# Performance work log

Hardware: AMD Instinct MI355X
Metric: run time of the kernel (lower is better)

## Reference

```python
import jax, jax.numpy as jnp
import numpy as np

TOPK = 8
NOISE_EPS = 0.01
_SQRT2 = np.sqrt(2.0).astype(np.float32)

def _norm_cdf(v):
    return 0.5 * (1.0 + jax.lax.erf(v / _SQRT2))

def setup_inputs() -> dict:
    key = jax.random.key(0)
    k1, k2, k3, k4 = jax.random.split(key, 4)
    B, D, E = 16384, 4096, 64
    return {
        "x": jax.random.normal(k1, (B, D), dtype=jnp.float32),
        "w_gate": jax.random.normal(k2, (D, E), dtype=jnp.float32) * 0.02,
        "w_noise": jax.random.normal(k3, (D, E), dtype=jnp.float32) * 0.02,
        "noise": jax.random.normal(k4, (B, E), dtype=jnp.float32),
    }

def reference(x, w_gate, w_noise, noise):
    B = x.shape[0]
    clean_logits = x @ w_gate                                   # [B, E]
    noise_stddev = jax.nn.softplus(x @ w_noise) + NOISE_EPS      # [B, E]
    noisy_logits = clean_logits + noise * noise_stddev           # [B, E]
    # NOTE: original applies softmax BEFORE topk (probabilities, not logits)
    probs = jax.nn.softmax(noisy_logits, axis=1)                 # [B, E]
    top_logits, top_indices = jax.lax.top_k(probs, TOPK + 1)     # [B, k+1]
    top_k_gates = jax.nn.softmax(top_logits[:, :TOPK], axis=1)   # [B, k]
    rows = jnp.arange(B)[:, None]
    gates = jnp.zeros_like(probs).at[rows, top_indices[:, :TOPK]].set(top_k_gates)
    # _prob_in_top_k: thresholds are the (topk)-th and (topk-1)-th top probs
    thr_in = top_logits[:, TOPK:TOPK + 1]                        # [B, 1]
    thr_out = top_logits[:, TOPK - 1:TOPK]                       # [B, 1]
    is_in = noisy_logits > thr_in                                # (faithful: raw noisy vs prob threshold)
    prob_if_in = _norm_cdf((clean_logits - thr_in) / noise_stddev)
    prob_if_out = _norm_cdf((clean_logits - thr_out) / noise_stddev)
    load = jnp.where(is_in, prob_if_in, prob_if_out).sum(axis=0)  # [E]
    return gates, load
```

## Files before the change

kernel.cpp:

```cpp
#include <hip/hip_runtime.h>
#include <math.h>

#define BB 16384
#define DD 4096
#define EE 64
#define TK 8

typedef __attribute__((ext_vector_type(8))) short s16x8;
typedef __attribute__((ext_vector_type(4))) float f32x4;

__device__ inline unsigned pack_hi2(float a, float b) {
    return (__float_as_uint(a) >> 16) | (__float_as_uint(b) & 0xFFFF0000u);
}
__device__ inline float hi_part(float a) {
    return __uint_as_float(__float_as_uint(a) & 0xFFFF0000u);
}

__global__ __launch_bounds__(256, 1)
void prep_w(const float* __restrict__ wg, const float* __restrict__ wn,
            char* __restrict__ wsB)
{
    __shared__ float Wtmp[64 * 132];
    const int t  = threadIdx.x;
    const int kc = blockIdx.x;

#pragma unroll
    for (int i = 0; i < 8; ++i) {
        int fid = t + i * 256;
        int m   = fid >> 10;
        int id  = fid & 1023;
        int kk  = id >> 4;
        int n4  = id & 15;
        const float* src = (m ? wn : wg) + (size_t)(kc * 64 + kk) * EE + n4 * 4;
        float4 v = *(const float4*)src;
        *(float4*)&Wtmp[kk * 132 + m * 64 + n4 * 4] = v;
    }
    __syncthreads();

#pragma unroll
    for (int i = 0; i < 4; ++i) {
        int id  = t + i * 256;
        int sub = id >> 9;
        int nt  = (id >> 6) & 7;
        int ln  = id & 63;
        int n   = nt * 16 + (ln & 15);
        int k0  = sub * 32 + (ln >> 4) * 8;
        float f[8];
#pragma unroll
        for (int j = 0; j < 8; ++j) f[j] = Wtmp[(k0 + j) * 132 + n];
        uint4 h, l;
        h.x = pack_hi2(f[0], f[1]); h.y = pack_hi2(f[2], f[3]);
        h.z = pack_hi2(f[4], f[5]); h.w = pack_hi2(f[6], f[7]);
        l.x = pack_hi2(f[0] - hi_part(f[0]), f[1] - hi_part(f[1]));
        l.y = pack_hi2(f[2] - hi_part(f[2]), f[3] - hi_part(f[3]));
        l.z = pack_hi2(f[4] - hi_part(f[4]), f[5] - hi_part(f[5]));
        l.w = pack_hi2(f[6] - hi_part(f[6]), f[7] - hi_part(f[7]));
        size_t base = (size_t)kc * 32768;
        *(uint4*)(wsB + base + (size_t)(((sub * 2 + 0) * 8 + nt) * 64 + ln) * 16) = h;
        *(uint4*)(wsB + base + (size_t)(((sub * 2 + 1) * 8 + nt) * 64 + ln) * 16) = l;
    }
}

__global__ __launch_bounds__(512, 1)
void moe_mfma(const float* __restrict__ x,
              const float* __restrict__ noise,
              const char* __restrict__ wsB,
              float* __restrict__ gates,
              float* __restrict__ load)
{
    __shared__ uint4 Afrag[1024];
    __shared__ uint4 Bfrag[2048];
    __shared__ float Ls[64 * 132];
    __shared__ float red[512];

    const int tid  = threadIdx.x;
    const int w    = tid >> 6;
    const int lane = tid & 63;
    const int wm   = w >> 1;
    const int wn   = w & 1;
    const int rb   = blockIdx.x * 64;

    const int srow  = tid >> 3;
    const int skg   = tid & 7;
    const int ssub  = skg >> 2;
    const int sq    = skg & 3;
    const int slane = sq * 16 + (srow & 15);
    const int smt   = srow >> 4;
    const int aoff_hi = ((ssub * 2 + 0) * 4 + smt) * 64 + slane;
    const int aoff_lo = ((ssub * 2 + 1) * 4 + smt) * 64 + slane;
    const float* xrow = x + (size_t)(rb + srow) * DD + skg * 8;

    f32x4 acc[4];
#pragma unroll
    for (int nt = 0; nt < 4; ++nt) acc[nt] = (f32x4){0.f, 0.f, 0.f, 0.f};

    for (int ch = 0; ch < DD / 64; ++ch) {
        float4 v0 = *(const float4*)(xrow + ch * 64);
        float4 v1 = *(const float4*)(xrow + ch * 64 + 4);

        const char* gB = wsB + (size_t)ch * 32768;
#pragma unroll
        for (int i = 0; i < 4; ++i) {
            const int si = w * 4 + i;
            __builtin_amdgcn_global_load_lds(
                (const __attribute__((address_space(1))) unsigned int*)(gB + (size_t)si * 1024 + lane * 16),
                (__attribute__((address_space(3))) unsigned int*)&Bfrag[si * 64],
                16, 0, 0);
        }

        uint4 h, l;
        h.x = pack_hi2(v0.x, v0.y); h.y = pack_hi2(v0.z, v0.w);
        h.z = pack_hi2(v1.x, v1.y); h.w = pack_hi2(v1.z, v1.w);
        l.x = pack_hi2(v0.x - hi_part(v0.x), v0.y - hi_part(v0.y));
        l.y = pack_hi2(v0.z - hi_part(v0.z), v0.w - hi_part(v0.w));
        l.z = pack_hi2(v1.x - hi_part(v1.x), v1.y - hi_part(v1.y));
        l.w = pack_hi2(v1.z - hi_part(v1.z), v1.w - hi_part(v1.w));
        Afrag[aoff_hi] = h;
        Afrag[aoff_lo] = l;
        __syncthreads();

#pragma unroll
        for (int sub = 0; sub < 2; ++sub) {
            const s16x8 ah = *(const s16x8*)&Afrag[((sub * 2 + 0) * 4 + wm) * 64 + lane];
            const s16x8 al = *(const s16x8*)&Afrag[((sub * 2 + 1) * 4 + wm) * 64 + lane];
#pragma unroll
            for (int nt = 0; nt < 4; ++nt) {
                const s16x8 bh = *(const s16x8*)&Bfrag[((sub * 2 + 0) * 8 + wn * 4 + nt) * 64 + lane];
                const s16x8 bl = *(const s16x8*)&Bfrag[((sub * 2 + 1) * 8 + wn * 4 + nt) * 64 + lane];
                acc[nt] = __builtin_amdgcn_mfma_f32_16x16x32_bf16(ah, bh, acc[nt], 0, 0, 0);
                acc[nt] = __builtin_amdgcn_mfma_f32_16x16x32_bf16(ah, bl, acc[nt], 0, 0, 0);
                acc[nt] = __builtin_amdgcn_mfma_f32_16x16x32_bf16(al, bh, acc[nt], 0, 0, 0);
            }
        }
        __syncthreads();
    }

    const int q4 = lane >> 4, cc = lane & 15;
#pragma unroll
    for (int nt = 0; nt < 4; ++nt)
#pragma unroll
        for (int r = 0; r < 4; ++r)
            Ls[(wm * 16 + q4 * 4 + r) * 132 + wn * 64 + nt * 16 + cc] = acc[nt][r];
    __syncthreads();

    float loadAcc = 0.f;
    for (int rr = 0; rr < 8; ++rr) {
        const int row = w * 8 + rr;
        const float clean = Ls[row * 132 + lane];
        const float rawn  = Ls[row * 132 + 64 + lane];
        const float nz    = noise[(size_t)(rb + row) * EE + lane];

        const float sp = fmaxf(rawn, 0.f) + log1pf(expf(-fabsf(rawn)));
        const float sd = sp + 0.01f;
        const float noisy = clean + nz * sd;

        float m = noisy;
#pragma unroll
        for (int off = 32; off; off >>= 1) m = fmaxf(m, __shfl_xor(m, off));
        const float ex = expf(noisy - m);
        float s = ex;
#pragma unroll
        for (int off = 32; off; off >>= 1) s += __shfl_xor(s, off);
        const float p = ex / s;

        float cur = p;
        int selrank = -1;
        float v[9];
#pragma unroll
        for (int j = 0; j < 9; ++j) {
            float bv = cur;
            int   bi = lane;
#pragma unroll
            for (int off = 32; off; off >>= 1) {
                const float ov = __shfl_xor(bv, off);
                const int   oi = __shfl_xor(bi, off);
                if (ov > bv || (ov == bv && oi < bi)) { bv = ov; bi = oi; }
            }
            v[j] = bv;
            if (lane == bi) { cur = -1.f; if (j < TK) selrank = j; }
        }

        float denom = 0.f;
#pragma unroll
        for (int j = 0; j < TK; ++j) denom += expf(v[j] - v[0]);
        const float gate = (selrank >= 0) ? (expf(p - v[0]) / denom) : 0.f;
        gates[(size_t)(rb + row) * EE + lane] = gate;

        const float thr_in  = v[8];
        const float thr_out = v[7];
        const bool  is_in   = noisy > thr_in;
        const float a = (clean - (is_in ? thr_in : thr_out)) / sd;
        loadAcc += 0.5f * (1.f + erff(a * 0.70710678118654752f));
    }

    red[w * 64 + lane] = loadAcc;
    __syncthreads();
    if (tid < 64) {
        float s = 0.f;
#pragma unroll
        for (int i = 0; i < 8; ++i) s += red[i * 64 + tid];
        atomicAdd(&load[tid], s);
    }
}

extern "C" void kernel_launch(void* const* d_in, const int* in_sizes, int n_in,
                              void* d_out, int out_size, void* d_ws, size_t ws_size,
                              hipStream_t stream)
{
    const float* x     = (const float*)d_in[0];
    const float* wg    = (const float*)d_in[1];
    const float* wn    = (const float*)d_in[2];
    const float* noise = (const float*)d_in[3];
    float* gates = (float*)d_out;
    float* load  = (float*)d_out + (size_t)BB * EE;
    char*  wsB   = (char*)d_ws;

    hipMemsetAsync(load, 0, EE * sizeof(float), stream);
    hipLaunchKernelGGL(prep_w, dim3(DD / 64), dim3(256), 0, stream, wg, wn, wsB);
    hipLaunchKernelGGL(moe_mfma, dim3(BB / 64), dim3(512), 0, stream,
                       x, noise, wsB, gates, load);
}
```

Baseline: 481.3 us.

## Double-buffer B tiles, load A straight to registers, use 4-wave blocks

The GEMM main loop now double-buffers the pre-split bf16 weight fragments in LDS and prefetches the next chunk's x values into registers while the current chunk is computed. The A operand is split into hi/lo bf16 directly in registers in MFMA layout, which removes the LDS staging and one barrier per chunk. The block shrinks to 4 waves, each computing two 16-row M tiles so the B fragments are reused. This is meant to hide global load latency and cut LDS traffic, at the cost of more registers per wave, fewer waves per block, and per-lane strided x loads.

```diff
diff --git a/kernel.cpp b/kernel.cpp
--- a/kernel.cpp
+++ b/kernel.cpp
@@ -14,6 +14,14 @@
 }
 __device__ inline float hi_part(float a) {
     return __uint_as_float(__float_as_uint(a) & 0xFFFF0000u);
+}
+__device__ inline void split_pack(const float4& v0, const float4& v1, uint4& h, uint4& l) {
+    h.x = pack_hi2(v0.x, v0.y); h.y = pack_hi2(v0.z, v0.w);
+    h.z = pack_hi2(v1.x, v1.y); h.w = pack_hi2(v1.z, v1.w);
+    l.x = pack_hi2(v0.x - hi_part(v0.x), v0.y - hi_part(v0.y));
+    l.y = pack_hi2(v0.z - hi_part(v0.z), v0.w - hi_part(v0.w));
+    l.z = pack_hi2(v1.x - hi_part(v1.x), v1.y - hi_part(v1.y));
+    l.w = pack_hi2(v1.z - hi_part(v1.z), v1.w - hi_part(v1.w));
 }
 
 __global__ __launch_bounds__(256, 1)
@@ -61,91 +69,107 @@
     }
 }
 
-__global__ __launch_bounds__(512, 1)
+__global__ __launch_bounds__(256, 1)
 void moe_mfma(const float* __restrict__ x,
               const float* __restrict__ noise,
               const char* __restrict__ wsB,
               float* __restrict__ gates,
               float* __restrict__ load)
 {
-    __shared__ uint4 Afrag[1024];
-    __shared__ uint4 Bfrag[2048];
-    __shared__ float Ls[64 * 132];
-    __shared__ float red[512];
+    __shared__ uint4 Bbuf[2][2048];
+    __shared__ float red[256];
 
     const int tid  = threadIdx.x;
     const int w    = tid >> 6;
     const int lane = tid & 63;
     const int wm   = w >> 1;
-    const int wn   = w & 1;
+    const int wnh  = w & 1;
     const int rb   = blockIdx.x * 64;
 
-    const int srow  = tid >> 3;
-    const int skg   = tid & 7;
-    const int ssub  = skg >> 2;
-    const int sq    = skg & 3;
-    const int slane = sq * 16 + (srow & 15);
-    const int smt   = srow >> 4;
-    const int aoff_hi = ((ssub * 2 + 0) * 4 + smt) * 64 + slane;
-    const int aoff_lo = ((ssub * 2 + 1) * 4 + smt) * 64 + slane;
-    const float* xrow = x + (size_t)(rb + srow) * DD + skg * 8;
-
-    f32x4 acc[4];
-#pragma unroll
-    for (int nt = 0; nt < 4; ++nt) acc[nt] = (f32x4){0.f, 0.f, 0.f, 0.f};
-
-    for (int ch = 0; ch < DD / 64; ++ch) {
-        float4 v0 = *(const float4*)(xrow + ch * 64);
-        float4 v1 = *(const float4*)(xrow + ch * 64 + 4);
-
+    const int m16 = lane & 15;
+    const int q   = lane >> 4;
+
+    const float* xbase = x + (size_t)(rb + wm * 32 + m16) * DD + q * 8;
+
+    f32x4 acc[2][4];
+#pragma unroll
+    for (int mt = 0; mt < 2; ++mt)
+#pragma unroll
+        for (int nt = 0; nt < 4; ++nt) acc[mt][nt] = (f32x4){0.f, 0.f, 0.f, 0.f};
+
+    auto issue_dma = [&](int ch, int b) {
         const char* gB = wsB + (size_t)ch * 32768;
 #pragma unroll
-        for (int i = 0; i < 4; ++i) {
-            const int si = w * 4 + i;
+        for (int i = 0; i < 8; ++i) {
+            const int si = w * 8 + i;
             __builtin_amdgcn_global_load_lds(
                 (const __attribute__((address_space(1))) unsigned int*)(gB + (size_t)si * 1024 + lane * 16),
-                (__attribute__((address_space(3))) unsigned int*)&Bfrag[si * 64],
+                (__attribute__((address_space(3))) unsigned int*)&Bbuf[b][si * 64],
                 16, 0, 0);
         }
-
-        uint4 h, l;
-        h.x = pack_hi2(v0.x, v0.y); h.y = pack_hi2(v0.z, v0.w);
-        h.z = pack_hi2(v1.x, v1.y); h.w = pack_hi2(v1.z, v1.w);
-        l.x = pack_hi2(v0.x - hi_part(v0.x), v0.y - hi_part(v0.y));
-        l.y = pack_hi2(v0.z - hi_part(v0.z), v0.w - hi_part(v0.w));
-        l.z = pack_hi2(v1.x - hi_part(v1.x), v1.y - hi_part(v1.y));
-        l.w = pack_hi2(v1.z - hi_part(v1.z), v1.w - hi_part(v1.w));
-        Afrag[aoff_hi] = h;
-        Afrag[aoff_lo] = l;
+    };
+    auto load_a = [&](int ch, float4* xv) {
+#pragma unroll
+        for (int mt = 0; mt < 2; ++mt)
+#pragma unroll
+            for (int sub = 0; sub < 2; ++sub) {
+                const float* p = xbase + (size_t)mt * 16 * DD + ch * 64 + sub * 32;
+                xv[(mt * 2 + sub) * 2 + 0] = *(const float4*)p;
+                xv[(mt * 2 + sub) * 2 + 1] = *(const float4*)(p + 4);
+            }
+    };
+    auto compute = [&](int b, const float4* xv) {
+#pragma unroll
+        for (int mt = 0; mt < 2; ++mt)
+#pragma unroll
+            for (int sub = 0; sub < 2; ++sub) {
+                uint4 h, l;
+                split_pack(xv[(mt * 2 + sub) * 2 + 0], xv[(mt * 2 + sub) * 2 + 1], h, l);
+                const s16x8 ah = __builtin_bit_cast(s16x8, h);
+                const s16x8 al = __builtin_bit_cast(s16x8, l);
+#pragma unroll
+                for (int nt = 0; nt < 4; ++nt) {
+                    const s16x8 bh = *(const s16x8*)&Bbuf[b][((sub * 2 + 0) * 8 + wnh * 4 + nt) * 64 + lane];
+                    const s16x8 bl = *(const s16x8*)&Bbuf[b][((sub * 2 + 1) * 8 + wnh * 4 + nt) * 64 + lane];
+                    acc[mt][nt] = __builtin_amdgcn_mfma_f32_16x16x32_bf16(ah, bh, acc[mt][nt], 0, 0, 0);
+                    acc[mt][nt] = __builtin_amdgcn_mfma_f32_16x16x32_bf16(ah, bl, acc[mt][nt], 0, 0, 0);
+                    acc[mt][nt] = __builtin_amdgcn_mfma_f32_16x16x32_bf16(al, bh, acc[mt][nt], 0, 0, 0);
+                }
+            }
+    };
+
+    float4 xva[8], xvb[8];
+    issue_dma(0, 0);
+    load_a(0, xva);
+
+    for (int ch = 0; ch < 64; ch += 2) {
         __syncthreads();
-
-#pragma unroll
-        for (int sub = 0; sub < 2; ++sub) {
-            const s16x8 ah = *(const s16x8*)&Afrag[((sub * 2 + 0) * 4 + wm) * 64 + lane];
-            const s16x8 al = *(const s16x8*)&Afrag[((sub * 2 + 1) * 4 + wm) * 64 + lane];
-#pragma unroll
-            for (int nt = 0; nt < 4; ++nt) {
-                const s16x8 bh = *(const s16x8*)&Bfrag[((sub * 2 + 0) * 8 + wn * 4 + nt) * 64 + lane];
-                const s16x8 bl = *(const s16x8*)&Bfrag[((sub * 2 + 1) * 8 + wn * 4 + nt) * 64 + lane];
-                acc[nt] = __builtin_amdgcn_mfma_f32_16x16x32_bf16(ah, bh, acc[nt], 0, 0, 0);
-                acc[nt] = __builtin_amdgcn_mfma_f32_16x16x32_bf16(ah, bl, acc[nt], 0, 0, 0);
-                acc[nt] = __builtin_amdgcn_mfma_f32_16x16x32_bf16(al, bh, acc[nt], 0, 0, 0);
-            }
+        issue_dma(ch + 1, 1);
+        load_a(ch + 1, xvb);
+        compute(0, xva);
+        __syncthreads();
+        if (ch + 2 < 64) {
+            issue_dma(ch + 2, 0);
+            load_a(ch + 2, xva);
         }
-        __syncthreads();
-    }
-
+        compute(1, xvb);
+    }
+
+    __syncthreads();
+    float* Ls = (float*)&Bbuf[0][0];
     const int q4 = lane >> 4, cc = lane & 15;
 #pragma unroll
-    for (int nt = 0; nt < 4; ++nt)
-#pragma unroll
-        for (int r = 0; r < 4; ++r)
-            Ls[(wm * 16 + q4 * 4 + r) * 132 + wn * 64 + nt * 16 + cc] = acc[nt][r];
+    for (int mt = 0; mt < 2; ++mt)
+#pragma unroll
+        for (int nt = 0; nt < 4; ++nt)
+#pragma unroll
+            for (int r = 0; r < 4; ++r)
+                Ls[(wm * 32 + mt * 16 + q4 * 4 + r) * 132 + wnh * 64 + nt * 16 + cc] = acc[mt][nt][r];
     __syncthreads();
 
     float loadAcc = 0.f;
-    for (int rr = 0; rr < 8; ++rr) {
-        const int row = w * 8 + rr;
+    for (int rr = 0; rr < 16; ++rr) {
+        const int row = w * 16 + rr;
         const float clean = Ls[row * 132 + lane];
         const float rawn  = Ls[row * 132 + 64 + lane];
         const float nz    = noise[(size_t)(rb + row) * EE + lane];
@@ -196,9 +220,7 @@
     red[w * 64 + lane] = loadAcc;
     __syncthreads();
     if (tid < 64) {
-        float s = 0.f;
-#pragma unroll
-        for (int i = 0; i < 8; ++i) s += red[i * 64 + tid];
+        const float s = red[tid] + red[64 + tid] + red[128 + tid] + red[192 + tid];
         atomicAdd(&load[tid], s);
     }
 }
@@ -217,6 +239,6 @@
 
     hipMemsetAsync(load, 0, EE * sizeof(float), stream);
     hipLaunchKernelGGL(prep_w, dim3(DD / 64), dim3(256), 0, stream, wg, wn, wsB);
-    hipLaunchKernelGGL(moe_mfma, dim3(BB / 64), dim3(512), 0, stream,
+    hipLaunchKernelGGL(moe_mfma, dim3(BB / 64), dim3(256), 0, stream,
                        x, noise, wsB, gates, load);
 }
```

After: 532.5 us. 10.6% more time.
